# Kernel optimization log

Measured on AMD Instinct MI355X. Metric: run time of the kernel, lower is better.

## Reference

```python
import jax, jax.numpy as jnp
import numpy as np

N = 1024
D_IN = 512
D = 128
E = 8192


def setup_inputs() -> dict:
    key = jax.random.key(0)
    ks = jax.random.split(key, 7)
    return {
        "inputs": jax.random.normal(ks[0], (N, D_IN), dtype=jnp.float32),
        "adj": jax.random.uniform(ks[1], (N, N), dtype=jnp.float32),
        "weight": jax.random.normal(ks[2], (D_IN, D), dtype=jnp.float32) * 0.05,
        "weight_two": jax.random.normal(ks[3], (2 * D, D), dtype=jnp.float32) * 0.05,
        "weight_three": jax.random.normal(ks[4], (2 * D, 1), dtype=jnp.float32) * 0.05,
        "train_edges": jax.random.randint(ks[5], (E, 2), 0, N, dtype=jnp.int64 if jax.config.jax_enable_x64 else jnp.int32),
        "train_false_edges": jax.random.randint(ks[6], (E, 2), 0, N, dtype=jnp.int64 if jax.config.jax_enable_x64 else jnp.int32),
    }


def reference(inputs, adj, weight, weight_two, weight_three, train_edges, train_false_edges):
    # encoder: x = X W ; z = A x   (single GCN-style layer, no bias)
    x = inputs @ weight          # (N, D)
    z = adj @ x                  # (N, D)
    n, d = z.shape

    # all-pairs features: pair (i, j) -> [z_i ; z_j]  (torch repeat/reshape semantics)
    z1 = jnp.broadcast_to(z[:, None, :], (n, n, d))   # z1[i,j] = z[i]
    z2 = jnp.broadcast_to(z[None, :, :], (n, n, d))   # z2[i,j] = z[j]

    z_pair = jax.nn.relu(jnp.concatenate([z1, z2], axis=-1))   # (N, N, 2D)
    z_pair = jnp.einsum('ijk,kl->ijl', z_pair, weight_two)     # (N, N, D)
    z_em = z1 * z2                                             # (N, N, D)

    score = jnp.einsum('ijk,kl->ijl', jnp.concatenate([z_pair, z_em], axis=-1), weight_three)
    return jax.nn.sigmoid(score[..., 0])  # (N, N)
```

## Files before the change

### kernel.cpp

```cpp
#include <hip/hip_runtime.h>
#include <math.h>

#define NN 1024
#define DIN 512
#define DD 128
#define NSPLIT 8

static constexpr long S = (long)NN * DD;
static constexpr long XP_OFF = 0;
static constexpr long ZP_OFF = XP_OFF + NSPLIT * S;
static constexpr long X_OFF  = ZP_OFF + NSPLIT * S;
static constexpr long Z_OFF  = X_OFF + S;
static constexpr long U_OFF  = Z_OFF + S;
static constexpr long A_OFF  = U_OFF + 256;
static constexpr long B_OFF  = A_OFF + NN;

__global__ __launch_bounds__(256) void gemm16(
    const float* __restrict__ A, const float* __restrict__ B,
    float* __restrict__ Cp, int K, int Kc,
    const float* __restrict__ W2, const float* __restrict__ w3,
    float* __restrict__ u) {
  if (blockIdx.y == NSPLIT) {
    if (blockIdx.x == 0) {
      const int kq = threadIdx.x;
      const float4* Wr = (const float4*)&W2[(long)kq * DD];
      float uu = 0.f;
#pragma unroll 8
      for (int l = 0; l < DD / 4; ++l) {
        const float4 wv = Wr[l];
        const float4 cv = ((const float4*)w3)[l];
        uu += wv.x * cv.x + wv.y * cv.y + wv.z * cv.z + wv.w * cv.w;
      }
      u[kq] = uu;
    }
    return;
  }

  const int t = threadIdx.x;
  const int tx = t & 31;
  const int ty = t >> 5;
  const int row0 = blockIdx.x * 16;
  const int k0 = blockIdx.y * Kc;

  float acc[2][4] = {};

  for (int k = k0; k < k0 + Kc; k += 4) {
    float4 bv[4];
#pragma unroll
    for (int kk = 0; kk < 4; ++kk)
      bv[kk] = *(const float4*)&B[(long)(k + kk) * DD + 4 * tx];
    float4 av[2];
#pragma unroll
    for (int mr = 0; mr < 2; ++mr)
      av[mr] = *(const float4*)&A[(long)(row0 + ty + 8 * mr) * K + k];
#pragma unroll
    for (int mr = 0; mr < 2; ++mr) {
      const float ar[4] = {av[mr].x, av[mr].y, av[mr].z, av[mr].w};
#pragma unroll
      for (int kk = 0; kk < 4; ++kk) {
        acc[mr][0] += ar[kk] * bv[kk].x;
        acc[mr][1] += ar[kk] * bv[kk].y;
        acc[mr][2] += ar[kk] * bv[kk].z;
        acc[mr][3] += ar[kk] * bv[kk].w;
      }
    }
  }

  float* Cs = Cp + (long)blockIdx.y * S;
#pragma unroll
  for (int mr = 0; mr < 2; ++mr) {
    const int r = row0 + ty + 8 * mr;
    *(float4*)&Cs[(long)r * DD + 4 * tx] =
        make_float4(acc[mr][0], acc[mr][1], acc[mr][2], acc[mr][3]);
  }
}

__global__ __launch_bounds__(256) void reduce_x(
    const float* __restrict__ xp, float* __restrict__ x) {
  const long i = (long)blockIdx.x * 256 + threadIdx.x;
  float s = 0.f;
#pragma unroll
  for (int p = 0; p < NSPLIT; ++p) s += xp[p * S + i];
  x[i] = s;
}

__global__ __launch_bounds__(128) void finalize_z(
    const float* __restrict__ zp, float* __restrict__ z,
    const float* __restrict__ u, float* __restrict__ a, float* __restrict__ b) {
  __shared__ float red[2][2];
  const int i = blockIdx.x;
  const int c = threadIdx.x;
  float s = 0.f;
#pragma unroll
  for (int p = 0; p < NSPLIT; ++p) s += zp[p * S + (long)i * DD + c];
  z[(long)i * DD + c] = s;

  const float r = s > 0.f ? s : 0.f;
  float pa = r * u[c];
  float pb = r * u[DD + c];
#pragma unroll
  for (int off = 32; off > 0; off >>= 1) {
    pa += __shfl_down(pa, off);
    pb += __shfl_down(pb, off);
  }
  const int w = c >> 6;
  if ((c & 63) == 0) { red[w][0] = pa; red[w][1] = pb; }
  __syncthreads();
  if (c == 0) {
    a[i] = red[0][0] + red[1][0];
    b[i] = red[0][1] + red[1][1];
  }
}

__global__ __launch_bounds__(256) void k4_decode(
    const float* __restrict__ z, const float* __restrict__ w3,
    const float* __restrict__ a, const float* __restrict__ b,
    float* __restrict__ out) {
  __shared__ float zwl[64 * DD];
  const int t = threadIdx.x;
  const int i0 = blockIdx.y * 32;
  const int j0 = blockIdx.x * 64;

#pragma unroll
  for (int s = 0; s < 8; ++s) {
    const int q = s * 256 + t;
    const int r = q >> 5;
    const int k4 = (q & 31) << 2;
    float4 w = *(const float4*)&z[(long)(j0 + r) * DD + k4];
    const float4 cc = *(const float4*)&w3[DD + k4];
    w.x *= cc.x; w.y *= cc.y; w.z *= cc.z; w.w *= cc.w;
    *(float4*)&zwl[r * DD + (k4 ^ ((r & 7) << 2))] = w;
  }
  __syncthreads();

  const int tx = t & 15;
  const int ty = t >> 4;
  float acc[2][4] = {};
  for (int k4 = 0; k4 < DD; k4 += 4) {
    float4 ar[2], bc[4];
#pragma unroll
    for (int m = 0; m < 2; ++m)
      ar[m] = *(const float4*)&z[(long)(i0 + ty + 16 * m) * DD + k4];
#pragma unroll
    for (int m = 0; m < 4; ++m) {
      const int C = tx + 16 * m;
      bc[m] = *(const float4*)&zwl[C * DD + (k4 ^ ((C & 7) << 2))];
    }
#pragma unroll
    for (int mr = 0; mr < 2; ++mr)
#pragma unroll
      for (int mc = 0; mc < 4; ++mc)
        acc[mr][mc] += ar[mr].x * bc[mc].x + ar[mr].y * bc[mc].y +
                       ar[mr].z * bc[mc].z + ar[mr].w * bc[mc].w;
  }

#pragma unroll
  for (int mr = 0; mr < 2; ++mr) {
    const int i = i0 + ty + 16 * mr;
    const float ai = a[i];
#pragma unroll
    for (int mc = 0; mc < 4; ++mc) {
      const int j = j0 + tx + 16 * mc;
      const float sc = ai + b[j] + acc[mr][mc];
      out[(long)i * NN + j] = 1.0f / (1.0f + __expf(-sc));
    }
  }
}

extern "C" void kernel_launch(void* const* d_in, const int* in_sizes, int n_in,
                              void* d_out, int out_size, void* d_ws, size_t ws_size,
                              hipStream_t stream) {
  (void)in_sizes; (void)n_in; (void)out_size; (void)ws_size;
  const float* inputs = (const float*)d_in[0];
  const float* adj    = (const float*)d_in[1];
  const float* weight = (const float*)d_in[2];
  const float* W2     = (const float*)d_in[3];
  const float* w3     = (const float*)d_in[4];
  float* out = (float*)d_out;

  float* ws = (float*)d_ws;
  float* xp = ws + XP_OFF;
  float* zp = ws + ZP_OFF;
  float* x  = ws + X_OFF;
  float* z  = ws + Z_OFF;
  float* u  = ws + U_OFF;
  float* a  = ws + A_OFF;
  float* b  = ws + B_OFF;

  gemm16<<<dim3(64, NSPLIT + 1), 256, 0, stream>>>(inputs, weight, xp, DIN,
                                                   DIN / NSPLIT, W2, w3, u);
  reduce_x<<<512, 256, 0, stream>>>(xp, x);
  gemm16<<<dim3(64, NSPLIT), 256, 0, stream>>>(adj, x, zp, NN, NN / NSPLIT,
                                               W2, w3, u);
  finalize_z<<<1024, 128, 0, stream>>>(zp, z, u, a, b);
  k4_decode<<<dim3(16, 32), 256, 0, stream>>>(z, w3, a, b, out);
}
```

Before: 109.3 us.

## Fuse split-K reductions and finalize into GEMM and decode kernels, cut launches

Replaces the five-kernel pipeline with three. The X GEMM now reduces its split-K partials in shared memory inside each block, and the adj GEMM uses a 4-way split. Summing the Z partials, the ReLU/u projection for a and b, and the z_i tile loads are all folded into the decode kernel's shared-memory staging. This removes two launches and the round trips for the partial buffers, z, a and b. In exchange, every decode block re-reduces its Z partial tiles redundantly, and the GEMMs lose register tiling because each thread now computes one output row.

Result: slower. 120.9 us (+10.6%).

```diff
diff --git a/kernel.cpp b/kernel.cpp
--- a/kernel.cpp
+++ b/kernel.cpp
@@ -4,119 +4,90 @@
 #define NN 1024
 #define DIN 512
 #define DD 128
-#define NSPLIT 8
+#define ZSPLIT 4
 
 static constexpr long S = (long)NN * DD;
-static constexpr long XP_OFF = 0;
-static constexpr long ZP_OFF = XP_OFF + NSPLIT * S;
-static constexpr long X_OFF  = ZP_OFF + NSPLIT * S;
-static constexpr long Z_OFF  = X_OFF + S;
-static constexpr long U_OFF  = Z_OFF + S;
-static constexpr long A_OFF  = U_OFF + 256;
-static constexpr long B_OFF  = A_OFF + NN;
+static constexpr long X_OFF  = 0;
+static constexpr long ZP_OFF = X_OFF + S;
+static constexpr long U_OFF  = ZP_OFF + ZSPLIT * S;
 
-__global__ __launch_bounds__(256) void gemm16(
-    const float* __restrict__ A, const float* __restrict__ B,
-    float* __restrict__ Cp, int K, int Kc,
+__global__ __launch_bounds__(256) void gemm_x(
+    const float* __restrict__ inputs, const float* __restrict__ weight,
     const float* __restrict__ W2, const float* __restrict__ w3,
-    float* __restrict__ u) {
-  if (blockIdx.y == NSPLIT) {
-    if (blockIdx.x == 0) {
-      const int kq = threadIdx.x;
-      const float4* Wr = (const float4*)&W2[(long)kq * DD];
-      float uu = 0.f;
+    float* __restrict__ x, float* __restrict__ u) {
+  if (blockIdx.x == 512) {
+    const int kq = threadIdx.x;
+    const float4* Wr = (const float4*)&W2[(long)kq * DD];
+    float uu = 0.f;
 #pragma unroll 8
-      for (int l = 0; l < DD / 4; ++l) {
-        const float4 wv = Wr[l];
-        const float4 cv = ((const float4*)w3)[l];
-        uu += wv.x * cv.x + wv.y * cv.y + wv.z * cv.z + wv.w * cv.w;
-      }
-      u[kq] = uu;
+    for (int l = 0; l < DD / 4; ++l) {
+      const float4 wv = Wr[l];
+      const float4 cv = ((const float4*)w3)[l];
+      uu += wv.x * cv.x + wv.y * cv.y + wv.z * cv.z + wv.w * cv.w;
     }
+    u[kq] = uu;
     return;
   }
 
+  __shared__ float4 part[256];
+  const int t = threadIdx.x;
+  const int cg = t & 31;
+  const int rw = (t >> 5) & 1;
+  const int kq = t >> 6;
+  const int row = blockIdx.x * 2 + rw;
+  const int k0 = kq * (DIN / 4);
+
+  float4 acc = make_float4(0.f, 0.f, 0.f, 0.f);
+  for (int k = k0; k < k0 + DIN / 4; k += 4) {
+    const float4 av = *(const float4*)&inputs[(long)row * DIN + k];
+    const float ar[4] = {av.x, av.y, av.z, av.w};
+#pragma unroll
+    for (int kk = 0; kk < 4; ++kk) {
+      const float4 bv = *(const float4*)&weight[(long)(k + kk) * DD + 4 * cg];
+      acc.x += ar[kk] * bv.x; acc.y += ar[kk] * bv.y;
+      acc.z += ar[kk] * bv.z; acc.w += ar[kk] * bv.w;
+    }
+  }
+  part[t] = acc;
+  __syncthreads();
+  if (kq == 0) {
+    const float4 p1 = part[t + 64], p2 = part[t + 128], p3 = part[t + 192];
+    acc.x += p1.x + p2.x + p3.x; acc.y += p1.y + p2.y + p3.y;
+    acc.z += p1.z + p2.z + p3.z; acc.w += p1.w + p2.w + p3.w;
+    *(float4*)&x[(long)row * DD + 4 * cg] = acc;
+  }
+}
+
+__global__ __launch_bounds__(256) void gemm_z(
+    const float* __restrict__ adj, const float* __restrict__ x,
+    float* __restrict__ zp) {
   const int t = threadIdx.x;
   const int tx = t & 31;
   const int ty = t >> 5;
-  const int row0 = blockIdx.x * 16;
-  const int k0 = blockIdx.y * Kc;
+  const int row = blockIdx.x * 8 + ty;
+  const int k0 = blockIdx.y * (NN / ZSPLIT);
 
-  float acc[2][4] = {};
-
-  for (int k = k0; k < k0 + Kc; k += 4) {
-    float4 bv[4];
+  float4 acc = make_float4(0.f, 0.f, 0.f, 0.f);
+  for (int k = k0; k < k0 + NN / ZSPLIT; k += 4) {
+    const float4 av = *(const float4*)&adj[(long)row * NN + k];
+    const float ar[4] = {av.x, av.y, av.z, av.w};
 #pragma unroll
-    for (int kk = 0; kk < 4; ++kk)
-      bv[kk] = *(const float4*)&B[(long)(k + kk) * DD + 4 * tx];
-    float4 av[2];
-#pragma unroll
-    for (int mr = 0; mr < 2; ++mr)
-      av[mr] = *(const float4*)&A[(long)(row0 + ty + 8 * mr) * K + k];
-#pragma unroll
-    for (int mr = 0; mr < 2; ++mr) {
-      const float ar[4] = {av[mr].x, av[mr].y, av[mr].z, av[mr].w};
-#pragma unroll
-      for (int kk = 0; kk < 4; ++kk) {
-        acc[mr][0] += ar[kk] * bv[kk].x;
-        acc[mr][1] += ar[kk] * bv[kk].y;
-        acc[mr][2] += ar[kk] * bv[kk].z;
-        acc[mr][3] += ar[kk] * bv[kk].w;
-      }
+    for (int kk = 0; kk < 4; ++kk) {
+      const float4 bv = *(const float4*)&x[(long)(k + kk) * DD + 4 * tx];
+      acc.x += ar[kk] * bv.x; acc.y += ar[kk] * bv.y;
+      acc.z += ar[kk] * bv.z; acc.w += ar[kk] * bv.w;
     }
   }
-
-  float* Cs = Cp + (long)blockIdx.y * S;
-#pragma unroll
-  for (int mr = 0; mr < 2; ++mr) {
-    const int r = row0 + ty + 8 * mr;
-    *(float4*)&Cs[(long)r * DD + 4 * tx] =
-        make_float4(acc[mr][0], acc[mr][1], acc[mr][2], acc[mr][3]);
-  }
-}
-
-__global__ __launch_bounds__(256) void reduce_x(
-    const float* __restrict__ xp, float* __restrict__ x) {
-  const long i = (long)blockIdx.x * 256 + threadIdx.x;
-  float s = 0.f;
-#pragma unroll
-  for (int p = 0; p < NSPLIT; ++p) s += xp[p * S + i];
-  x[i] = s;
-}
-
-__global__ __launch_bounds__(128) void finalize_z(
-    const float* __restrict__ zp, float* __restrict__ z,
-    const float* __restrict__ u, float* __restrict__ a, float* __restrict__ b) {
-  __shared__ float red[2][2];
-  const int i = blockIdx.x;
-  const int c = threadIdx.x;
-  float s = 0.f;
-#pragma unroll
-  for (int p = 0; p < NSPLIT; ++p) s += zp[p * S + (long)i * DD + c];
-  z[(long)i * DD + c] = s;
-
-  const float r = s > 0.f ? s : 0.f;
-  float pa = r * u[c];
-  float pb = r * u[DD + c];
-#pragma unroll
-  for (int off = 32; off > 0; off >>= 1) {
-    pa += __shfl_down(pa, off);
-    pb += __shfl_down(pb, off);
-  }
-  const int w = c >> 6;
-  if ((c & 63) == 0) { red[w][0] = pa; red[w][1] = pb; }
-  __syncthreads();
-  if (c == 0) {
-    a[i] = red[0][0] + red[1][0];
-    b[i] = red[0][1] + red[1][1];
-  }
+  *(float4*)&zp[(long)blockIdx.y * S + (long)row * DD + 4 * tx] = acc;
 }
 
 __global__ __launch_bounds__(256) void k4_decode(
-    const float* __restrict__ z, const float* __restrict__ w3,
-    const float* __restrict__ a, const float* __restrict__ b,
-    float* __restrict__ out) {
+    const float* __restrict__ zp, const float* __restrict__ w3,
+    const float* __restrict__ u, float* __restrict__ out) {
   __shared__ float zwl[64 * DD];
+  __shared__ float zil[32 * DD];
+  __shared__ float a_loc[32];
+  __shared__ float b_loc[64];
   const int t = threadIdx.x;
   const int i0 = blockIdx.y * 32;
   const int j0 = blockIdx.x * 64;
@@ -126,10 +97,41 @@
     const int q = s * 256 + t;
     const int r = q >> 5;
     const int k4 = (q & 31) << 2;
-    float4 w = *(const float4*)&z[(long)(j0 + r) * DD + k4];
+    float4 sum = make_float4(0.f, 0.f, 0.f, 0.f);
+#pragma unroll
+    for (int p = 0; p < ZSPLIT; ++p) {
+      const float4 v = *(const float4*)&zp[(long)p * S + (long)(j0 + r) * DD + k4];
+      sum.x += v.x; sum.y += v.y; sum.z += v.z; sum.w += v.w;
+    }
+    const float4 uv = *(const float4*)&u[DD + k4];
+    float bp = fmaxf(sum.x, 0.f) * uv.x + fmaxf(sum.y, 0.f) * uv.y +
+               fmaxf(sum.z, 0.f) * uv.z + fmaxf(sum.w, 0.f) * uv.w;
+#pragma unroll
+    for (int off = 16; off > 0; off >>= 1) bp += __shfl_down(bp, off, 32);
+    if ((t & 31) == 0) b_loc[r] = bp;
     const float4 cc = *(const float4*)&w3[DD + k4];
-    w.x *= cc.x; w.y *= cc.y; w.z *= cc.z; w.w *= cc.w;
-    *(float4*)&zwl[r * DD + (k4 ^ ((r & 7) << 2))] = w;
+    sum.x *= cc.x; sum.y *= cc.y; sum.z *= cc.z; sum.w *= cc.w;
+    *(float4*)&zwl[r * DD + (k4 ^ ((r & 7) << 2))] = sum;
+  }
+
+#pragma unroll
+  for (int s = 0; s < 4; ++s) {
+    const int q = s * 256 + t;
+    const int r = q >> 5;
+    const int k4 = (q & 31) << 2;
+    float4 sum = make_float4(0.f, 0.f, 0.f, 0.f);
+#pragma unroll
+    for (int p = 0; p < ZSPLIT; ++p) {
+      const float4 v = *(const float4*)&zp[(long)p * S + (long)(i0 + r) * DD + k4];
+      sum.x += v.x; sum.y += v.y; sum.z += v.z; sum.w += v.w;
+    }
+    const float4 uv = *(const float4*)&u[k4];
+    float ap = fmaxf(sum.x, 0.f) * uv.x + fmaxf(sum.y, 0.f) * uv.y +
+               fmaxf(sum.z, 0.f) * uv.z + fmaxf(sum.w, 0.f) * uv.w;
+#pragma unroll
+    for (int off = 16; off > 0; off >>= 1) ap += __shfl_down(ap, off, 32);
+    if ((t & 31) == 0) a_loc[r] = ap;
+    *(float4*)&zil[r * DD + (k4 ^ ((r & 7) << 2))] = sum;
   }
   __syncthreads();
 
@@ -139,8 +141,10 @@
   for (int k4 = 0; k4 < DD; k4 += 4) {
     float4 ar[2], bc[4];
 #pragma unroll
-    for (int m = 0; m < 2; ++m)
-      ar[m] = *(const float4*)&z[(long)(i0 + ty + 16 * m) * DD + k4];
+    for (int m = 0; m < 2; ++m) {
+      const int R = ty + 16 * m;
+      ar[m] = *(const float4*)&zil[R * DD + (k4 ^ ((R & 7) << 2))];
+    }
 #pragma unroll
     for (int m = 0; m < 4; ++m) {
       const int C = tx + 16 * m;
@@ -157,11 +161,11 @@
 #pragma unroll
   for (int mr = 0; mr < 2; ++mr) {
     const int i = i0 + ty + 16 * mr;
-    const float ai = a[i];
+    const float ai = a_loc[ty + 16 * mr];
 #pragma unroll
     for (int mc = 0; mc < 4; ++mc) {
       const int j = j0 + tx + 16 * mc;
-      const float sc = ai + b[j] + acc[mr][mc];
+      const float sc = ai + b_loc[tx + 16 * mc] + acc[mr][mc];
       out[(long)i * NN + j] = 1.0f / (1.0f + __expf(-sc));
     }
   }
@@ -179,19 +183,11 @@
   float* out = (float*)d_out;
 
   float* ws = (float*)d_ws;
-  float* xp = ws + XP_OFF;
+  float* x  = ws + X_OFF;
   float* zp = ws + ZP_OFF;
-  float* x  = ws + X_OFF;
-  float* z  = ws + Z_OFF;
   float* u  = ws + U_OFF;
-  float* a  = ws + A_OFF;
-  float* b  = ws + B_OFF;
 
-  gemm16<<<dim3(64, NSPLIT + 1), 256, 0, stream>>>(inputs, weight, xp, DIN,
-                                                   DIN / NSPLIT, W2, w3, u);
-  reduce_x<<<512, 256, 0, stream>>>(xp, x);
-  gemm16<<<dim3(64, NSPLIT), 256, 0, stream>>>(adj, x, zp, NN, NN / NSPLIT,
-                                               W2, w3, u);
-  finalize_z<<<1024, 128, 0, stream>>>(zp, z, u, a, b);
-  k4_decode<<<dim3(16, 32), 256, 0, stream>>>(z, w3, a, b, out);
+  gemm_x<<<513, 256, 0, stream>>>(inputs, weight, W2, w3, x, u);
+  gemm_z<<<dim3(128, ZSPLIT), 256, 0, stream>>>(adj, x, zp);
+  k4_decode<<<dim3(16, 32), 256, 0, stream>>>(zp, w3, u, out);
 }
```
